# Performance work log

Measured on AMD Instinct MI355X. Metric: run time of the kernel, lower is better.

Reference implementation:

```python
import jax, jax.numpy as jnp
import numpy as np

N = 8192       # number of tokens/nodes (in_dim)
D = 128        # feature dim (out_dim)
R_BASE = 40    # number of dependency labels; reverse doubles it


def setup_inputs() -> dict:
    key = jax.random.key(0)
    ks = jax.random.split(key, 8)
    x = jax.random.normal(ks[0], (N, D), dtype=jnp.float32)
    # 'self' linear (applied to every node)
    W_self = jax.random.normal(ks[1], (D, D), dtype=jnp.float32) / np.sqrt(D)
    b_self = jax.random.normal(ks[2], (D,), dtype=jnp.float32) * 0.01
    # relation-specific linears: [0, R_BASE) forward labels, [R_BASE, 2*R_BASE) reversed labels
    W_rel = jax.random.normal(ks[3], (2 * R_BASE, D, D), dtype=jnp.float32) / np.sqrt(D)
    b_rel = jax.random.normal(ks[4], (2 * R_BASE, D), dtype=jnp.float32) * 0.01
    # dependency triples (dependent=dst, label=rel, governor=src), one edge per token
    src = jax.random.randint(ks[5], (N,), 0, N)
    dst = jax.random.randint(ks[6], (N,), 0, N)
    rel = jax.random.randint(ks[7], (N,), 0, R_BASE)
    return dict(x=x, W_self=W_self, b_self=b_self, W_rel=W_rel, b_rel=b_rel,
                src=src, dst=dst, rel=rel)


def reference(x, W_self, b_self, W_rel, b_rel, src, dst, rel):
    n = x.shape[0]
    # self-loop transform: temp_tensor[idx] = self(x[idx])
    out = x @ W_self.T + b_self
    # reverse_case=True: each triple contributes
    #   out[dst] += W[rel] @ x[src] + b[rel]
    #   out[src] += W[rel + R_BASE] @ x[dst] + b[rel + R_BASE]
    src_all = jnp.concatenate([src, dst])           # [2E]
    dst_all = jnp.concatenate([dst, src])           # [2E]
    rel_all = jnp.concatenate([rel, rel + R_BASE])  # [2E]
    # gather per-edge relation matrix and apply (nn.Linear: y = W @ v + b)
    msgs = jnp.einsum('edk,ek->ed', W_rel[rel_all], x[src_all]) + b_rel[rel_all]
    out = out + jax.ops.segment_sum(msgs, dst_all, num_segments=n)
    return out
```

## Files before the change

kernel.cpp:

```cpp
#include <hip/hip_runtime.h>
#include <hip/hip_bf16.h>

#define D 128
#define RBASE 40
#define NREL 80
#define NR1 81
#define TILE 64
#define CAP 1024
#define TPR (CAP / TILE)

typedef __attribute__((ext_vector_type(8))) short short8;
typedef __attribute__((ext_vector_type(4))) float f32x4;

static __device__ __forceinline__ unsigned short f2bf(float f) {
    unsigned int u = __float_as_uint(f);
    u += 0x7FFF + ((u >> 16) & 1);
    return (unsigned short)(u >> 16);
}
static __device__ __forceinline__ float bf2f(unsigned short h) {
    return __uint_as_float(((unsigned int)h) << 16);
}

__global__ __launch_bounds__(1024) void prep_fused(
        const int* __restrict__ src, const int* __restrict__ dst,
        const float* __restrict__ Wr, const float* __restrict__ Ws,
        const float* __restrict__ x,
        int* __restrict__ cur_rel, int* __restrict__ off_dst,
        int* __restrict__ cur_dst,
        unsigned short* __restrict__ Wbf, unsigned short* __restrict__ xbf,
        int ne, int nn) {
    const int b = blockIdx.x;
    const int t = threadIdx.x;

    if (b == 0) {
        __shared__ int cnt[8192];
        __shared__ int woff[16];
        const int lane = t & 63;
        const int wid  = t >> 6;

        for (int i = t; i < nn; i += 1024) cnt[i] = 0;
        if (t < 128) cur_rel[t] = 0;
        __syncthreads();

        const int etot = 2 * ne;
        for (int e = t; e < etot; e += 1024) {
            int d = (e < ne) ? dst[e] : src[e - ne];
            atomicAdd(&cnt[d], 1);
        }
        __syncthreads();

        const int CH = (nn + 1023) / 1024;
        const int base = t * CH;
        int segs[8];
        int ssum = 0;
        #pragma unroll
        for (int i = 0; i < 8; ++i) {
            int idx = base + i;
            int v = (i < CH && idx < nn) ? (cnt[idx] + 1) : 0;
            segs[i] = v;
            ssum += v;
        }
        int inc = ssum;
        for (int dd = 1; dd < 64; dd <<= 1) {
            int v = __shfl_up(inc, dd);
            if (lane >= dd) inc += v;
        }
        if (lane == 63) woff[wid] = inc;
        __syncthreads();
        if (t < 16) {
            int v = woff[t];
            int wi = v;
            for (int dd = 1; dd < 16; dd <<= 1) {
                int u = __shfl_up(wi, dd);
                if (lane >= dd) wi += u;
            }
            woff[t] = wi - v;
        }
        __syncthreads();
        int off = woff[wid] + (inc - ssum);
        #pragma unroll
        for (int i = 0; i < 8; ++i) {
            int idx = base + i;
            if (i < CH && idx < nn) {
                off_dst[idx] = off;
                cur_dst[idx] = off + 1;
                off += segs[i];
            }
        }
        if (t == 1023) off_dst[nn] = off;
    } else {
        const int wq = NR1 * D * D / 4;
        const int xq = nn * D / 4;
        const int tq = wq + xq;
        const int stride = (gridDim.x - 1) * 1024;
        for (int i = (b - 1) * 1024 + t; i < tq; i += stride) {
            float4 v;
            unsigned short* op;
            if (i < wq) {
                int e0 = i * 4;
                const float* sp = (e0 < NREL * D * D) ? (Wr + e0)
                                                      : (Ws + (e0 - NREL * D * D));
                v  = *reinterpret_cast<const float4*>(sp);
                op = Wbf + e0;
            } else {
                int e0 = (i - wq) * 4;
                v  = *reinterpret_cast<const float4*>(x + e0);
                op = xbf + e0;
            }
            ushort4 o;
            o.x = f2bf(v.x); o.y = f2bf(v.y); o.z = f2bf(v.z); o.w = f2bf(v.w);
            *reinterpret_cast<ushort4*>(op) = o;
        }
    }
}

__global__ __launch_bounds__(1024) void scatter_kernel(
        const int* __restrict__ src, const int* __restrict__ dst,
        const int* __restrict__ rel,
        int* __restrict__ cur_rel, int* __restrict__ cur_dst,
        int* __restrict__ rb_src, int* __restrict__ rb_ds, int ne) {
    __shared__ int hrel[NREL];
    __shared__ int base_s[NREL];
    const int t = threadIdx.x;
    if (t < NREL) hrel[t] = 0;
    __syncthreads();

    const int e    = blockIdx.x * 1024 + t;
    const int etot = 2 * ne;
    int r = 0, d = 0, sn = 0, myslot = -1;
    if (e < etot) {
        if (e < ne) { r = rel[e];              d = dst[e];      sn = src[e];      }
        else        { r = rel[e - ne] + RBASE; d = src[e - ne]; sn = dst[e - ne]; }
        myslot = atomicAdd(&hrel[r], 1);
    }
    __syncthreads();
    if (t < NREL && hrel[t] > 0)
        base_s[t] = atomicAdd(cur_rel + t, hrel[t]);
    __syncthreads();
    if (e < etot) {
        int slot = base_s[r] + myslot;
        int pd   = atomicAdd(cur_dst + d, 1);
        if (slot < CAP) {
            rb_src[r * CAP + slot] = sn;
            rb_ds[r * CAP + slot]  = pd;
        }
    }
}

__global__ __launch_bounds__(256) void edge_mfma(
        const unsigned short* __restrict__ xbf,
        const unsigned short* __restrict__ Wbf,
        const float* __restrict__ br, const float* __restrict__ bs,
        const int* __restrict__ cur_rel,
        const int* __restrict__ rb_src, const int* __restrict__ rb_ds,
        const int* __restrict__ off_dst,
        unsigned short* __restrict__ msg, int nn) {
    __shared__ short Wl[D * D];
    __shared__ short Xl[TILE * D];
    __shared__ int   sEn[TILE];
    __shared__ int   dS[TILE];

    const int bid = blockIdx.x;
    int r, mr, s0 = 0, v0 = 0;
    bool selfp = false;
    if (bid < NREL * TPR) {
        r = bid / TPR;
        const int t = bid % TPR;
        int cnt = cur_rel[r];
        if (cnt > CAP) cnt = CAP;
        mr = cnt - t * TILE;
        if (mr <= 0) return;
        if (mr > TILE) mr = TILE;
        s0 = r * CAP + t * TILE;
    } else {
        selfp = true;
        r  = NREL;
        v0 = (bid - NREL * TPR) * TILE;
        mr = nn - v0;
        if (mr <= 0) return;
        if (mr > TILE) mr = TILE;
    }

    const int tid  = threadIdx.x;
    const int lane = tid & 63;
    const int wid  = tid >> 6;

    if (tid < TILE) {
        int s = -1, dsv = -1;
        if (tid < mr) {
            if (selfp) { s = v0 + tid;        dsv = off_dst[v0 + tid]; }
            else       { s = rb_src[s0 + tid]; dsv = rb_ds[s0 + tid];  }
        }
        sEn[tid] = s;
        dS[tid]  = dsv;
    }

    const unsigned short* Wp = Wbf + (size_t)r * D * D;
    #pragma unroll
    for (int j = 0; j < 8; ++j) {
        int c   = tid + j * 256;
        int row = c >> 4;
        int sc  = (c & 15) ^ (row & 7);
        uint4 v = *reinterpret_cast<const uint4*>(Wp + row * D + sc * 8);
        *reinterpret_cast<uint4*>(&Wl[c * 8]) = v;
    }
    __syncthreads();

    #pragma unroll
    for (int j = 0; j < 4; ++j) {
        int c    = tid + j * 256;
        int row  = c >> 4;
        int sc   = (c & 15) ^ (row & 7);
        int node = sEn[row];
        short8 o = {0, 0, 0, 0, 0, 0, 0, 0};
        if (node >= 0)
            o = *reinterpret_cast<const short8*>(xbf + (size_t)node * D + sc * 8);
        *reinterpret_cast<short8*>(&Xl[c * 8]) = o;
    }
    __syncthreads();

    const int q   = lane >> 4;
    const int l15 = lane & 15;

    f32x4 acc[2][4];
    #pragma unroll
    for (int mf = 0; mf < 2; ++mf)
        #pragma unroll
        for (int nf = 0; nf < 4; ++nf)
            acc[mf][nf] = (f32x4){0.f, 0.f, 0.f, 0.f};

    #pragma unroll
    for (int ks = 0; ks < 4; ++ks) {
        short8 a[2], b[4];
        #pragma unroll
        for (int mf = 0; mf < 2; ++mf) {
            int row = (wid * 2 + mf) * 16 + l15;
            int pc  = (ks * 4 + q) ^ (row & 7);
            a[mf] = *reinterpret_cast<const short8*>(&Wl[row * D + pc * 8]);
        }
        #pragma unroll
        for (int nf = 0; nf < 4; ++nf) {
            int er = nf * 16 + l15;
            int pc = (ks * 4 + q) ^ (er & 7);
            b[nf] = *reinterpret_cast<const short8*>(&Xl[er * D + pc * 8]);
        }
        #pragma unroll
        for (int mf = 0; mf < 2; ++mf)
            #pragma unroll
            for (int nf = 0; nf < 4; ++nf)
                acc[mf][nf] = __builtin_amdgcn_mfma_f32_16x16x32_bf16(
                    a[mf], b[nf], acc[mf][nf], 0, 0, 0);
    }

    const float* bp = (r == NREL) ? bs : (br + (size_t)r * D);
    #pragma unroll
    for (int mf = 0; mf < 2; ++mf) {
        int j0 = (wid * 2 + mf) * 16 + q * 4;
        float4 bias = *reinterpret_cast<const float4*>(bp + j0);
        #pragma unroll
        for (int nf = 0; nf < 4; ++nf) {
            int e  = nf * 16 + l15;
            int ds = dS[e];
            if (ds >= 0) {
                f32x4 v = acc[mf][nf];
                unsigned int lo = (unsigned int)f2bf(v[0] + bias.x) |
                                  ((unsigned int)f2bf(v[1] + bias.y) << 16);
                unsigned int hi = (unsigned int)f2bf(v[2] + bias.z) |
                                  ((unsigned int)f2bf(v[3] + bias.w) << 16);
                *reinterpret_cast<uint2*>(msg + (size_t)ds * D + j0) =
                    make_uint2(lo, hi);
            }
        }
    }
}

__global__ void gather_kernel(const unsigned short* __restrict__ msg,
                              const int* __restrict__ off_dst,
                              float* __restrict__ out, int nn) {
    const int tid = threadIdx.x;
    const int v   = blockIdx.x * 8 + (tid >> 5);
    const int j   = tid & 31;
    if (v >= nn) return;
    const int a = off_dst[v];
    const int b = off_dst[v + 1];
    float a0 = 0.f, a1 = 0.f, a2 = 0.f, a3 = 0.f;
    for (int s = a; s < b; ++s) {
        ushort4 m = *reinterpret_cast<const ushort4*>(msg + (size_t)s * D + j * 4);
        a0 += bf2f(m.x); a1 += bf2f(m.y); a2 += bf2f(m.z); a3 += bf2f(m.w);
    }
    *reinterpret_cast<float4*>(out + (size_t)v * D + j * 4) =
        make_float4(a0, a1, a2, a3);
}

extern "C" void kernel_launch(void* const* d_in, const int* in_sizes, int n_in,
                              void* d_out, int out_size, void* d_ws, size_t ws_size,
                              hipStream_t stream) {
    const float* x   = (const float*)d_in[0];
    const float* Ws  = (const float*)d_in[1];
    const float* bs  = (const float*)d_in[2];
    const float* Wr  = (const float*)d_in[3];
    const float* br  = (const float*)d_in[4];
    const int*   src = (const int*)d_in[5];
    const int*   dst = (const int*)d_in[6];
    const int*   rel = (const int*)d_in[7];
    float*       out = (float*)d_out;

    const int ne = in_sizes[5];
    const int nn = in_sizes[0] / D;
    if (ne <= 0 || nn <= 0) return;

    int* IW = (int*)d_ws;
    int* cur_rel  = IW;
    int* off_dst  = IW + 128;
    int* cur_dst  = off_dst + nn + 1;
    int* rb_src   = cur_dst + nn;
    int* rb_ds    = rb_src + NREL * CAP;
    size_t ofs = (size_t)((char*)(rb_ds + NREL * CAP) - (char*)d_ws);
    ofs = (ofs + 15) & ~(size_t)15;
    unsigned short* Wbf = (unsigned short*)((char*)d_ws + ofs);
    ofs += (size_t)NR1 * D * D * 2;
    unsigned short* xbf = (unsigned short*)((char*)d_ws + ofs);
    ofs += (size_t)nn * D * 2;
    unsigned short* msg = (unsigned short*)((char*)d_ws + ofs);

    prep_fused<<<128, 1024, 0, stream>>>(src, dst, Wr, Ws, x,
                                         cur_rel, off_dst, cur_dst,
                                         Wbf, xbf, ne, nn);

    scatter_kernel<<<(2 * ne + 1023) / 1024, 1024, 0, stream>>>(
        src, dst, rel, cur_rel, cur_dst, rb_src, rb_ds, ne);

    const int nblk = NREL * TPR + (nn + TILE - 1) / TILE;
    edge_mfma<<<nblk, 256, 0, stream>>>(xbf, Wbf, br, bs, cur_rel,
                                        rb_src, rb_ds, off_dst, msg, nn);

    gather_kernel<<<(nn + 7) / 8, 256, 0, stream>>>(msg, off_dst, out, nn);
}
```

Measured before the change: 48.01 us.

## Fold edge scatter into single-block prep, removing the scatter kernel launch

```diff
diff --git a/kernel.cpp b/kernel.cpp
--- a/kernel.cpp
+++ b/kernel.cpp
@@ -23,10 +23,11 @@
 
 __global__ __launch_bounds__(1024) void prep_fused(
         const int* __restrict__ src, const int* __restrict__ dst,
+        const int* __restrict__ rel,
         const float* __restrict__ Wr, const float* __restrict__ Ws,
         const float* __restrict__ x,
         int* __restrict__ cur_rel, int* __restrict__ off_dst,
-        int* __restrict__ cur_dst,
+        int* __restrict__ rb_src, int* __restrict__ rb_ds,
         unsigned short* __restrict__ Wbf, unsigned short* __restrict__ xbf,
         int ne, int nn) {
     const int b = blockIdx.x;
@@ -34,15 +35,16 @@
 
     if (b == 0) {
         __shared__ int cnt[8192];
+        __shared__ int hrel[NREL];
         __shared__ int woff[16];
         const int lane = t & 63;
         const int wid  = t >> 6;
+        const int etot = 2 * ne;
 
         for (int i = t; i < nn; i += 1024) cnt[i] = 0;
-        if (t < 128) cur_rel[t] = 0;
-        __syncthreads();
-
-        const int etot = 2 * ne;
+        if (t < NREL) hrel[t] = 0;
+        __syncthreads();
+
         for (int e = t; e < etot; e += 1024) {
             int d = (e < ne) ? dst[e] : src[e - ne];
             atomicAdd(&cnt[d], 1);
@@ -83,11 +85,27 @@
             int idx = base + i;
             if (i < CH && idx < nn) {
                 off_dst[idx] = off;
-                cur_dst[idx] = off + 1;
+                cnt[idx] = off + 1;
                 off += segs[i];
             }
         }
         if (t == 1023) off_dst[nn] = off;
+        __syncthreads();
+
+        for (int e = t; e < etot; e += 1024) {
+            int r, d, sn;
+            if (e < ne) { r = rel[e];              d = dst[e];      sn = src[e];      }
+            else        { r = rel[e - ne] + RBASE; d = src[e - ne]; sn = dst[e - ne]; }
+            int slot = atomicAdd(&hrel[r], 1);
+            int pd   = atomicAdd(&cnt[d], 1);
+            if (slot < CAP) {
+                rb_src[r * CAP + slot] = sn;
+                rb_ds[r * CAP + slot]  = pd;
+            }
+        }
+        __syncthreads();
+
+        if (t < NREL) cur_rel[t] = hrel[t];
     } else {
         const int wq = NR1 * D * D / 4;
         const int xq = nn * D / 4;
@@ -110,39 +128,6 @@
             ushort4 o;
             o.x = f2bf(v.x); o.y = f2bf(v.y); o.z = f2bf(v.z); o.w = f2bf(v.w);
             *reinterpret_cast<ushort4*>(op) = o;
-        }
-    }
-}
-
-__global__ __launch_bounds__(1024) void scatter_kernel(
-        const int* __restrict__ src, const int* __restrict__ dst,
-        const int* __restrict__ rel,
-        int* __restrict__ cur_rel, int* __restrict__ cur_dst,
-        int* __restrict__ rb_src, int* __restrict__ rb_ds, int ne) {
-    __shared__ int hrel[NREL];
-    __shared__ int base_s[NREL];
-    const int t = threadIdx.x;
-    if (t < NREL) hrel[t] = 0;
-    __syncthreads();
-
-    const int e    = blockIdx.x * 1024 + t;
-    const int etot = 2 * ne;
-    int r = 0, d = 0, sn = 0, myslot = -1;
-    if (e < etot) {
-        if (e < ne) { r = rel[e];              d = dst[e];      sn = src[e];      }
-        else        { r = rel[e - ne] + RBASE; d = src[e - ne]; sn = dst[e - ne]; }
-        myslot = atomicAdd(&hrel[r], 1);
-    }
-    __syncthreads();
-    if (t < NREL && hrel[t] > 0)
-        base_s[t] = atomicAdd(cur_rel + t, hrel[t]);
-    __syncthreads();
-    if (e < etot) {
-        int slot = base_s[r] + myslot;
-        int pd   = atomicAdd(cur_dst + d, 1);
-        if (slot < CAP) {
-            rb_src[r * CAP + slot] = sn;
-            rb_ds[r * CAP + slot]  = pd;
         }
     }
 }
@@ -312,8 +297,7 @@
     int* IW = (int*)d_ws;
     int* cur_rel  = IW;
     int* off_dst  = IW + 128;
-    int* cur_dst  = off_dst + nn + 1;
-    int* rb_src   = cur_dst + nn;
+    int* rb_src   = off_dst + nn + 1;
     int* rb_ds    = rb_src + NREL * CAP;
     size_t ofs = (size_t)((char*)(rb_ds + NREL * CAP) - (char*)d_ws);
     ofs = (ofs + 15) & ~(size_t)15;
@@ -323,12 +307,9 @@
     ofs += (size_t)nn * D * 2;
     unsigned short* msg = (unsigned short*)((char*)d_ws + ofs);
 
-    prep_fused<<<128, 1024, 0, stream>>>(src, dst, Wr, Ws, x,
-                                         cur_rel, off_dst, cur_dst,
+    prep_fused<<<128, 1024, 0, stream>>>(src, dst, rel, Wr, Ws, x,
+                                         cur_rel, off_dst, rb_src, rb_ds,
                                          Wbf, xbf, ne, nn);
-
-    scatter_kernel<<<(2 * ne + 1023) / 1024, 1024, 0, stream>>>(
-        src, dst, rel, cur_rel, cur_dst, rb_src, rb_ds, ne);
 
     const int nblk = NREL * TPR + (nn + TILE - 1) / TILE;
     edge_mfma<<<nblk, 256, 0, stream>>>(xbf, Wbf, br, bs, cur_rel,
```

New measurement: 55.11 us. +14.8%, slower.
